# Performance work log

Measured on AMD Instinct MI355X. Metric: run time of the kernel, lower is better.

The kernel has to match this reference:

```python
import jax, jax.numpy as jnp
import numpy as np

D_MODEL = 1024
HEADS = 16
D_K = D_MODEL // HEADS
B, S = 2, 2048


def setup_inputs() -> dict:
    key = jax.random.key(0)
    ks = jax.random.split(key, 11)
    sc = 1.0 / np.sqrt(D_MODEL)
    inp = {
        "q": jax.random.normal(ks[0], (B, S, D_MODEL), jnp.float32),
        "k": jax.random.normal(ks[1], (B, S, D_MODEL), jnp.float32),
        "v": jax.random.normal(ks[2], (B, S, D_MODEL), jnp.float32),
        # causal mask, broadcastable to (B, H, S, S); 0 -> masked
        "mask": jnp.tril(jnp.ones((S, S), jnp.int32))[None, None],
        "w_q": jax.random.normal(ks[3], (D_MODEL, D_MODEL), jnp.float32) * sc,
        "b_q": jax.random.normal(ks[4], (D_MODEL,), jnp.float32) * sc,
        "w_k": jax.random.normal(ks[5], (D_MODEL, D_MODEL), jnp.float32) * sc,
        "b_k": jax.random.normal(ks[6], (D_MODEL,), jnp.float32) * sc,
        "w_v": jax.random.normal(ks[7], (D_MODEL, D_MODEL), jnp.float32) * sc,
        "b_v": jax.random.normal(ks[8], (D_MODEL,), jnp.float32) * sc,
        "w_o": jax.random.normal(ks[9], (D_MODEL, D_MODEL), jnp.float32) * sc,
        "b_o": jax.random.normal(ks[10], (D_MODEL,), jnp.float32) * sc,
    }
    return inp


def reference(q, k, v, mask, w_q, b_q, w_k, b_k, w_v, b_v, w_o, b_o):
    b = q.shape[0]
    # torch Linear: x @ W.T + b
    Q = q @ w_q.T + b_q
    K = k @ w_k.T + b_k
    V = v @ w_v.T + b_v
    # (B, S, D) -> (B, H, S, d_k)
    Q = Q.reshape(b, -1, HEADS, D_K).transpose(0, 2, 1, 3)
    K = K.reshape(b, -1, HEADS, D_K).transpose(0, 2, 1, 3)
    V = V.reshape(b, -1, HEADS, D_K).transpose(0, 2, 1, 3)
    scores = jnp.einsum("bhqd,bhkd->bhqk", Q, K) / np.sqrt(D_K).astype(np.float32)
    scores = jnp.where(mask == 0, -jnp.inf, scores)
    attn = jax.nn.softmax(scores, axis=-1)
    out = jnp.einsum("bhqk,bhkd->bhqd", attn, V)
    out = out.transpose(0, 2, 1, 3).reshape(b, -1, D_MODEL)
    # dropout is identity in eval mode
    return out @ w_o.T + b_o
```

## Files before the change

### kernel.cpp

```cpp
#include <hip/hip_runtime.h>
#include <math.h>

#define D_MODEL 1024
#define N_HEADS 16
#define DKH     64
#define BATCH   2
#define SEQ     2048
#define NT128   (SEQ/128)
#define PARTS_PER_BH 40

typedef unsigned short u16;
typedef __attribute__((ext_vector_type(8))) short short8;
typedef __attribute__((ext_vector_type(4))) float f32x4;

__device__ __forceinline__ u16 f2bf(float f) {
    unsigned u = __float_as_uint(f);
    u += 0x7fffu + ((u >> 16) & 1u);
    return (u16)(u >> 16);
}
__device__ __forceinline__ float bf2f(u16 x) {
    return __int_as_float(((int)x) << 16);
}

__device__ __forceinline__ void gll16(const void* g, void* l) {
    __builtin_amdgcn_global_load_lds((const __attribute__((address_space(1))) void*)g,
                                     (__attribute__((address_space(3))) void*)l, 16, 0, 0);
}

template<int CTRL>
__device__ __forceinline__ float rormax(float x) {
    int r = __builtin_amdgcn_update_dpp(__float_as_int(x), __float_as_int(x),
                                        CTRL, 0xf, 0xf, false);
    return fmaxf(x, __int_as_float(r));
}
__device__ __forceinline__ float rowmax16(float x) {
    x = rormax<0x121>(x);
    x = rormax<0x122>(x);
    x = rormax<0x124>(x);
    x = rormax<0x128>(x);
    return x;
}

__global__ __launch_bounds__(256)
void convert_kernel(const float* __restrict__ q, const float* __restrict__ k,
                    const float* __restrict__ v, const float* __restrict__ wq,
                    const float* __restrict__ wk, const float* __restrict__ wv,
                    const float* __restrict__ wo,
                    u16* __restrict__ qb, u16* __restrict__ kb, u16* __restrict__ vb,
                    u16* __restrict__ wqb, u16* __restrict__ wkb,
                    u16* __restrict__ wvb, u16* __restrict__ wob)
{
    const size_t NV = ((size_t)16 << 20) >> 3;
    for (size_t i = (size_t)blockIdx.x * blockDim.x + threadIdx.x; i < NV;
         i += (size_t)gridDim.x * blockDim.x) {
        const size_t e = i << 3;
        const float* s; u16* d; size_t off;
        if (e < ((size_t)12 << 20)) {
            const int seg = (int)(e >> 22);
            off = e & (((size_t)1 << 22) - 1);
            s = seg == 0 ? q : seg == 1 ? k : v;
            d = seg == 0 ? qb : seg == 1 ? kb : vb;
        } else {
            const size_t r = e - ((size_t)12 << 20);
            const int seg = (int)(r >> 20);
            off = r & (((size_t)1 << 20) - 1);
            s = seg == 0 ? wq : seg == 1 ? wk : seg == 2 ? wv : wo;
            d = seg == 0 ? wqb : seg == 1 ? wkb : seg == 2 ? wvb : wob;
        }
        const float4 f0 = *(const float4*)(s + off);
        const float4 f1 = *(const float4*)(s + off + 4);
        short8 o;
        o[0]=(short)f2bf(f0.x); o[1]=(short)f2bf(f0.y); o[2]=(short)f2bf(f0.z); o[3]=(short)f2bf(f0.w);
        o[4]=(short)f2bf(f1.x); o[5]=(short)f2bf(f1.y); o[6]=(short)f2bf(f1.z); o[7]=(short)f2bf(f1.w);
        *(short8*)(d + off) = o;
    }
}

#define GEMM_PREAMBLE                                                            \
    __shared__ __align__(16) u16 As[2][128][32];                                 \
    __shared__ __align__(16) u16 Bs[2][128][32];                                 \
    const int tid  = threadIdx.x;                                                \
    const int lane = tid & 63;                                                   \
    const int wid  = tid >> 6;                                                   \
    const int wm   = wid >> 1, wn = wid & 1;                                     \
    const int lr   = lane & 15, lg = lane >> 4;                                  \
    const int mb   = blockIdx.x * 128, nb = blockIdx.y * 128;                    \
    const int g_row = lane >> 2;                                                 \
    const int g_col = (lane & 3) << 3;                                           \
    const u16* Ab = A  + (size_t)mb * K;                                         \
    const u16* Bb = Bw + (size_t)nb * K;                                         \
    f32x4 acc[4][4];                                                             \
    _Pragma("unroll")                                                            \
    for (int i = 0; i < 4; ++i)                                                  \
        _Pragma("unroll")                                                        \
        for (int j = 0; j < 4; ++j) { f32x4 z = {0.f,0.f,0.f,0.f}; acc[i][j] = z; }

#define STAGE(buf, kt)                                                           \
    {                                                                            \
        _Pragma("unroll")                                                        \
        for (int t = 0; t < 2; ++t) {                                            \
            const int r0 = t*64 + wid*16;                                        \
            gll16(&Ab[(size_t)(r0 + g_row)*K + (kt) + g_col], &As[buf][r0][0]);  \
            gll16(&Bb[(size_t)(r0 + g_row)*K + (kt) + g_col], &Bs[buf][r0][0]);  \
        }                                                                        \
    }

#define GEMM_MAINLOOP                                                            \
    STAGE(0, 0)                                                                  \
    __syncthreads();                                                             \
    const int NK = K >> 5;                                                       \
    for (int it = 0; it < NK; ++it) {                                            \
        const int c = it & 1;                                                    \
        if (it + 1 < NK) STAGE(c ^ 1, (it + 1) << 5)                             \
        short8 a[4], b[4];                                                       \
        _Pragma("unroll")                                                        \
        for (int i = 0; i < 4; ++i) a[i] = *(const short8*)&As[c][wm*64 + i*16 + lr][lg*8]; \
        _Pragma("unroll")                                                        \
        for (int j = 0; j < 4; ++j) b[j] = *(const short8*)&Bs[c][wn*64 + j*16 + lr][lg*8]; \
        _Pragma("unroll")                                                        \
        for (int i = 0; i < 4; ++i)                                              \
            _Pragma("unroll")                                                    \
            for (int j = 0; j < 4; ++j)                                          \
                acc[i][j] = __builtin_amdgcn_mfma_f32_16x16x32_bf16(a[i], b[j], acc[i][j], 0, 0, 0); \
        __syncthreads();                                                         \
    }

__global__ __launch_bounds__(256, 3)
void gemm_qkv_kernel(const u16* __restrict__ qb, const u16* __restrict__ kb,
                     const u16* __restrict__ vb, const u16* __restrict__ wqb,
                     const u16* __restrict__ wkb, const u16* __restrict__ wvb,
                     const float* __restrict__ b_q, const float* __restrict__ b_k,
                     const float* __restrict__ b_v,
                     u16* __restrict__ Qh, u16* __restrict__ Kh, u16* __restrict__ Vt,
                     int M, int N, int K)
{
    const int z = blockIdx.z;
    const u16* A    = z == 0 ? qb  : z == 1 ? kb  : vb;
    const u16* Bw   = z == 0 ? wqb : z == 1 ? wkb : wvb;
    const float* bias = z == 0 ? b_q : z == 1 ? b_k : b_v;
    u16* dst        = z == 0 ? Qh  : z == 1 ? Kh  : Vt;
    const float scale = z == 0 ? 0.125f : 1.0f;

    GEMM_PREAMBLE
    GEMM_MAINLOOP

    #pragma unroll
    for (int i = 0; i < 4; ++i) {
        #pragma unroll
        for (int j = 0; j < 4; ++j) {
            const int mbase = mb + wm*64 + i*16 + lg*4;
            const int n     = nb + wn*64 + j*16 + lr;
            const float bn  = bias[n];
            const int h = n >> 6, d = n & 63;
            #pragma unroll
            for (int r = 0; r < 4; ++r) {
                const int m = mbase + r;
                const int b = m >> 11, s = m & (SEQ - 1);
                const float val = (acc[i][j][r] + bn) * scale;
                if (z == 2)
                    dst[(((size_t)(b*N_HEADS + h))*DKH + d)*SEQ + s] = f2bf(val);
                else
                    dst[(((size_t)(b*N_HEADS + h))*SEQ + s)*DKH + d] = f2bf(val);
            }
        }
    }
}

__global__ __launch_bounds__(256)
void gemm_out_kernel(const u16* __restrict__ A, const u16* __restrict__ Bw,
                     const float* __restrict__ bias, float* __restrict__ dst,
                     int M, int N, int K)
{
    __shared__ __align__(16) u16 As[2][128][32];
    __shared__ __align__(16) u16 Bs[2][64][32];

    const int tid  = threadIdx.x;
    const int lane = tid & 63;
    const int wid  = tid >> 6;
    const int wm   = wid >> 1, wn = wid & 1;
    const int lr   = lane & 15, lg = lane >> 4;
    const int mb   = blockIdx.x * 128, nb = blockIdx.y * 64;
    const int g_row = lane >> 2;
    const int g_col = (lane & 3) << 3;

    const u16* Ab = A  + (size_t)mb * K;
    const u16* Bb = Bw + (size_t)nb * K;

    f32x4 acc[4][2];
    #pragma unroll
    for (int i = 0; i < 4; ++i)
        #pragma unroll
        for (int j = 0; j < 2; ++j) { f32x4 z = {0.f,0.f,0.f,0.f}; acc[i][j] = z; }

#define OSTAGE(buf, kt)                                                          \
    {                                                                            \
        _Pragma("unroll")                                                        \
        for (int t = 0; t < 2; ++t) {                                            \
            const int r0 = t*64 + wid*16;                                        \
            gll16(&Ab[(size_t)(r0 + g_row)*K + (kt) + g_col], &As[buf][r0][0]);  \
        }                                                                        \
        gll16(&Bb[(size_t)(wid*16 + g_row)*K + (kt) + g_col], &Bs[buf][wid*16][0]); \
    }

    OSTAGE(0, 0)
    __syncthreads();

    const int NK = K >> 5;
    for (int it = 0; it < NK; ++it) {
        const int c = it & 1;
        if (it + 1 < NK) OSTAGE(c ^ 1, (it + 1) << 5)

        short8 a[4], b[2];
        #pragma unroll
        for (int i = 0; i < 4; ++i) a[i] = *(const short8*)&As[c][wm*64 + i*16 + lr][lg*8];
        #pragma unroll
        for (int j = 0; j < 2; ++j) b[j] = *(const short8*)&Bs[c][wn*32 + j*16 + lr][lg*8];
        #pragma unroll
        for (int i = 0; i < 4; ++i)
            #pragma unroll
            for (int j = 0; j < 2; ++j)
                acc[i][j] = __builtin_amdgcn_mfma_f32_16x16x32_bf16(a[i], b[j], acc[i][j], 0, 0, 0);

        __syncthreads();
    }
#undef OSTAGE

    #pragma unroll
    for (int i = 0; i < 4; ++i) {
        #pragma unroll
        for (int j = 0; j < 2; ++j) {
            const int mbase = mb + wm*64 + i*16 + lg*4;
            const int n     = nb + wn*32 + j*16 + lr;
            const float bn  = bias[n];
            #pragma unroll
            for (int r = 0; r < 4; ++r)
                dst[(size_t)(mbase + r) * N + n] = acc[i][j][r] + bn;
        }
    }
}

__device__ __forceinline__ void attn_step(
    const short8& aq0, const short8& aq1,
    f32x4 (&o)[4], f32x4& osum, float (&m_run)[4],
    const u16 (*__restrict__ Kl)[64], const u16 (*__restrict__ Vl)[64],
    u16 (*__restrict__ Pw)[72],
    int kvb, int qbw, int lr, int lg)
{
    const int ksw = (lr & 7) << 3;
    f32x4 s[4];
    __builtin_amdgcn_s_setprio(1);
    #pragma unroll
    for (int cb = 0; cb < 4; ++cb) {
        const int kr = cb*16 + lr;
        f32x4 z = {0.f,0.f,0.f,0.f};
        short8 k0 = *(const short8*)&Kl[kr][( 0 + lg*8) ^ ksw];
        short8 k1 = *(const short8*)&Kl[kr][(32 + lg*8) ^ ksw];
        z = __builtin_amdgcn_mfma_f32_16x16x32_bf16(aq0, k0, z, 0, 0, 0);
        z = __builtin_amdgcn_mfma_f32_16x16x32_bf16(aq1, k1, z, 0, 0, 0);
        s[cb] = z;
    }
    __builtin_amdgcn_s_setprio(0);

    if (kvb + 63 > qbw) {
        #pragma unroll
        for (int cb = 0; cb < 4; ++cb)
            #pragma unroll
            for (int r = 0; r < 4; ++r)
                if (kvb + cb*16 + lr > qbw + lg*4 + r) s[cb][r] = -INFINITY;
    }

    float tm[4];
    #pragma unroll
    for (int r = 0; r < 4; ++r)
        tm[r] = rowmax16(fmaxf(fmaxf(s[0][r], s[1][r]), fmaxf(s[2][r], s[3][r])));

    int need = 0;
    #pragma unroll
    for (int r = 0; r < 4; ++r) need |= (tm[r] > m_run[r] + 8.f) ? 1 : 0;
    if (__any(need)) {
        #pragma unroll
        for (int r = 0; r < 4; ++r) {
            const float mnew  = fmaxf(m_run[r], tm[r]);
            const float alpha = __expf(m_run[r] - mnew);
            m_run[r] = mnew;
            osum[r] *= alpha;
            #pragma unroll
            for (int db = 0; db < 4; ++db) o[db][r] *= alpha;
        }
    }
    #pragma unroll
    for (int r = 0; r < 4; ++r)
        #pragma unroll
        for (int cb = 0; cb < 4; ++cb)
            Pw[lg*4 + r][cb*16 + lr] = f2bf(__expf(s[cb][r] - m_run[r]));

    short8 vone;
    #pragma unroll
    for (int j = 0; j < 8; ++j) vone[j] = (short)0x3F80;
    __builtin_amdgcn_s_setprio(1);
    #pragma unroll
    for (int ks = 0; ks < 2; ++ks) {
        short8 ap = *(short8*)&Pw[lr][ks*32 + lg*8];
        #pragma unroll
        for (int db = 0; db < 4; ++db) {
            const int vr = db*16 + lr;
            short8 bv = *(const short8*)&Vl[vr][(ks*32 + lg*8) ^ ksw];
            o[db] = __builtin_amdgcn_mfma_f32_16x16x32_bf16(ap, bv, o[db], 0, 0, 0);
        }
        osum = __builtin_amdgcn_mfma_f32_16x16x32_bf16(ap, vone, osum, 0, 0, 0);
    }
    __builtin_amdgcn_s_setprio(0);
}

__global__ __launch_bounds__(512)
void flash_split_kernel(const u16* __restrict__ Qh, const u16* __restrict__ Kh,
                        const u16* __restrict__ Vt, u16* __restrict__ part_o,
                        float* __restrict__ part_ms)
{
    __shared__ __align__(16) u16 Kl[64][64];
    __shared__ __align__(16) u16 Vl[64][64];
    __shared__ __align__(16) u16 P[8][16][72];

    const int x = blockIdx.x;
    int t, ch;
    if      (x <  4) { t = x;                 ch = 0;        }
    else if (x < 12) { t = 4 + ((x-4) >> 1);  ch = (x-4)&1;  }
    else if (x < 24) { t = 8 + (x-12)/3;      ch = (x-12)%3; }
    else             { t = 12 + ((x-24) >> 2); ch = (x-24)&3; }

    const int tid  = threadIdx.x;
    const int lane = tid & 63;
    const int wid  = tid >> 6;
    const int lr   = lane & 15, lg = lane >> 4;
    const int bh   = blockIdx.y;
    const int qbw  = t*128 + wid*16;
    const size_t base = (size_t)bh * SEQ * DKH;

    const int c0      = ch * 8;
    const int nc_here = min(8, 2*(t+1) - c0);

    const int srow = tid >> 3;
    const int se0  = (tid & 7) << 3;
    const int sec  = se0 ^ ((srow & 7) << 3);

    short8 aq0 = *(const short8*)&Qh[base + (size_t)(qbw + lr)*DKH +  0 + lg*8];
    short8 aq1 = *(const short8*)&Qh[base + (size_t)(qbw + lr)*DKH + 32 + lg*8];

    f32x4 o[4], osum;
    float m_run[4];
    #pragma unroll
    for (int r = 0; r < 4; ++r) m_run[r] = -INFINITY;
    {
        f32x4 z = {0.f,0.f,0.f,0.f};
        osum = z;
        #pragma unroll
        for (int db = 0; db < 4; ++db) o[db] = z;
    }

    {
        const int kb0 = c0 * 64;
        short8 k0 = *(const short8*)&Kh[base + (size_t)(kb0 + srow)*DKH + se0];
        short8 v0 = *(const short8*)&Vt[base + (size_t)srow*SEQ + kb0 + se0];
        *(short8*)&Kl[srow][sec] = k0;
        *(short8*)&Vl[srow][sec] = v0;
    }
    __syncthreads();

    for (int ci = 0; ci < nc_here; ++ci) {
        const int kvb = (c0 + ci) * 64;
        short8 nk0, nv0;
        const bool pref = (ci + 1 < nc_here);
        if (pref) {
            const int nb_ = kvb + 64;
            nk0 = *(const short8*)&Kh[base + (size_t)(nb_ + srow)*DKH + se0];
            nv0 = *(const short8*)&Vt[base + (size_t)srow*SEQ + nb_ + se0];
        }

        if (kvb <= qbw + 15)
            attn_step(aq0, aq1, o, osum, m_run, Kl, Vl, P[wid], kvb, qbw, lr, lg);

        __syncthreads();
        if (pref) {
            *(short8*)&Kl[srow][sec] = nk0;
            *(short8*)&Vl[srow][sec] = nv0;
        }
        __syncthreads();
    }

    const size_t slot = (size_t)bh * PARTS_PER_BH + x;
    u16*   po = part_o  + (slot << 13);
    float* pm = part_ms + (slot << 8);
    #pragma unroll
    for (int db = 0; db < 4; ++db)
        #pragma unroll
        for (int r = 0; r < 4; ++r)
            po[(wid*16 + lg*4 + r)*64 + db*16 + lr] = f2bf(o[db][r]);
    if (lr == 0) {
        #pragma unroll
        for (int r = 0; r < 4; ++r) {
            pm[(wid*16 + lg*4 + r)*2 + 0] = m_run[r];
            pm[(wid*16 + lg*4 + r)*2 + 1] = osum[r];
        }
    }
}

__global__ __launch_bounds__(256)
void merge_kernel(const u16* __restrict__ part_o, const float* __restrict__ part_ms,
                  u16* __restrict__ attb)
{
    const int t   = blockIdx.x;
    const int bh  = blockIdx.y;
    const int nch = min(4, (2*(t+1) + 7) >> 3);
    const int basex = t < 4 ? t : t < 8 ? 4 + 2*(t-4) : t < 12 ? 12 + 3*(t-8) : 24 + 4*(t-12);

    const int row = threadIdx.x >> 1;
    const int cb  = (threadIdx.x & 1) * 32;

    float mm[4], ss[4];
    float M = -INFINITY;
    for (int c = 0; c < nch; ++c) {
        const size_t slot = (size_t)bh * PARTS_PER_BH + basex + c;
        mm[c] = part_ms[(slot << 8) + row*2 + 0];
        ss[c] = part_ms[(slot << 8) + row*2 + 1];
        M = fmaxf(M, mm[c]);
    }
    float S = 0.f;
    float acc[32];
    #pragma unroll
    for (int j = 0; j < 32; ++j) acc[j] = 0.f;
    for (int c = 0; c < nch; ++c) {
        const float w = __expf(mm[c] - M);
        S += w * ss[c];
        const size_t slot = (size_t)bh * PARTS_PER_BH + basex + c;
        const u16* po = part_o + (slot << 13) + row*64 + cb;
        #pragma unroll
        for (int g = 0; g < 4; ++g) {
            short8 v = *(const short8*)(po + g*8);
            #pragma unroll
            for (int j = 0; j < 8; ++j)
                acc[g*8 + j] += w * bf2f((u16)v[j]);
        }
    }
    const float inv = 1.f / S;
    const int b = bh >> 4, h = bh & 15;
    const int grow = t*128 + row;
    u16* dst = attb + ((size_t)(b*SEQ + grow))*D_MODEL + h*64 + cb;
    #pragma unroll
    for (int g = 0; g < 4; ++g) {
        short8 ov;
        #pragma unroll
        for (int j = 0; j < 8; ++j) ov[j] = (short)f2bf(acc[g*8 + j] * inv);
        *(short8*)(dst + g*8) = ov;
    }
}

extern "C" void kernel_launch(void* const* d_in, const int* in_sizes, int n_in,
                              void* d_out, int out_size, void* d_ws, size_t ws_size,
                              hipStream_t stream)
{
    const float* q   = (const float*)d_in[0];
    const float* k   = (const float*)d_in[1];
    const float* v   = (const float*)d_in[2];
    const float* w_q = (const float*)d_in[4];
    const float* b_q = (const float*)d_in[5];
    const float* w_k = (const float*)d_in[6];
    const float* b_k = (const float*)d_in[7];
    const float* w_v = (const float*)d_in[8];
    const float* b_v = (const float*)d_in[9];
    const float* w_o = (const float*)d_in[10];
    const float* b_o = (const float*)d_in[11];

    char* ws = (char*)d_ws;
    const size_t MB = 1024*1024;
    u16* Qh   = (u16*)(ws +  0*MB);
    u16* Kh   = (u16*)(ws +  8*MB);
    u16* Vt   = (u16*)(ws + 16*MB);
    u16* qb   = (u16*)(ws + 24*MB);
    u16* kb   = (u16*)(ws + 32*MB);
    u16* vb   = (u16*)(ws + 40*MB);
    u16* wqb  = (u16*)(ws + 48*MB);
    u16* wkb  = (u16*)(ws + 50*MB);
    u16* wvb  = (u16*)(ws + 52*MB);
    u16* wob  = (u16*)(ws + 54*MB);
    u16* attb = qb;
    u16*   part_o  = (u16*)(ws + 32*MB);
    float* part_ms = (float*)(ws + 52*MB);

    const int M = BATCH * SEQ, N = D_MODEL, K = D_MODEL;

    convert_kernel<<<2048, 256, 0, stream>>>(q, k, v, w_q, w_k, w_v, w_o,
                                             qb, kb, vb, wqb, wkb, wvb, wob);
    gemm_qkv_kernel<<<dim3(M/128, N/128, 3), 256, 0, stream>>>(
        qb, kb, vb, wqb, wkb, wvb, b_q, b_k, b_v, Qh, Kh, Vt, M, N, K);
    flash_split_kernel<<<dim3(PARTS_PER_BH, BATCH*N_HEADS), 512, 0, stream>>>(
        Qh, Kh, Vt, part_o, part_ms);
    merge_kernel<<<dim3(NT128, BATCH*N_HEADS), 256, 0, stream>>>(part_o, part_ms, attb);
    gemm_out_kernel<<<dim3(M/128, N/64), 256, 0, stream>>>(attb, wob, b_o, (float*)d_out, M, N, K);
}
```

Baseline: 139.8 us.

## Compute transposed S tile so P feeds PV MFMA from registers

The attention step now computes S transposed (K as the A operand), so each lane holds one query row's scores across 16 keys. This allows row max via two cross-lane shuffles and lets P be packed into bf16 registers with v_cvt_pk_bf16_f32, feeding 16x16x16 MFMAs directly instead of going through an LDS round trip. The row sum is accumulated in scalar FP32 instead of a ones-vector MFMA. In exchange it uses twice as many smaller-K PV MFMAs, needs shuffles to broadcast the rescale alpha, and loads V with 8-byte LDS reads.

```diff
diff --git a/kernel.cpp b/kernel.cpp
--- a/kernel.cpp
+++ b/kernel.cpp
@@ -10,7 +10,9 @@
 #define PARTS_PER_BH 40
 
 typedef unsigned short u16;
+typedef unsigned long long u64;
 typedef __attribute__((ext_vector_type(8))) short short8;
+typedef __attribute__((ext_vector_type(4))) short s4v;
 typedef __attribute__((ext_vector_type(4))) float f32x4;
 
 __device__ __forceinline__ u16 f2bf(float f) {
@@ -27,18 +29,16 @@
                                      (__attribute__((address_space(3))) void*)l, 16, 0, 0);
 }
 
-template<int CTRL>
-__device__ __forceinline__ float rormax(float x) {
-    int r = __builtin_amdgcn_update_dpp(__float_as_int(x), __float_as_int(x),
-                                        CTRL, 0xf, 0xf, false);
-    return fmaxf(x, __int_as_float(r));
-}
-__device__ __forceinline__ float rowmax16(float x) {
-    x = rormax<0x121>(x);
-    x = rormax<0x122>(x);
-    x = rormax<0x124>(x);
-    x = rormax<0x128>(x);
-    return x;
+__device__ __forceinline__ f32x4 mfma16(s4v a, s4v b, f32x4 c) {
+#if __has_builtin(__builtin_amdgcn_mfma_f32_16x16x16bf16_1k)
+    return __builtin_amdgcn_mfma_f32_16x16x16bf16_1k(a, b, c, 0, 0, 0);
+#elif __has_builtin(__builtin_amdgcn_mfma_f32_16x16x16_bf16)
+    return __builtin_amdgcn_mfma_f32_16x16x16_bf16(a, b, c, 0, 0, 0);
+#else
+    f32x4 d;
+    asm("v_mfma_f32_16x16x16_bf16 %0, %1, %2, %3" : "=v"(d) : "v"(a), "v"(b), "v"(c));
+    return d;
+#endif
 }
 
 __global__ __launch_bounds__(256)
@@ -241,73 +241,82 @@
 
 __device__ __forceinline__ void attn_step(
     const short8& aq0, const short8& aq1,
-    f32x4 (&o)[4], f32x4& osum, float (&m_run)[4],
+    f32x4 (&o)[4], float& osum, float& m_run,
     const u16 (*__restrict__ Kl)[64], const u16 (*__restrict__ Vl)[64],
-    u16 (*__restrict__ Pw)[72],
     int kvb, int qbw, int lr, int lg)
 {
     const int ksw = (lr & 7) << 3;
-    f32x4 s[4];
+    f32x4 st[4];
     __builtin_amdgcn_s_setprio(1);
     #pragma unroll
-    for (int cb = 0; cb < 4; ++cb) {
-        const int kr = cb*16 + lr;
+    for (int c = 0; c < 4; ++c) {
+        const int kr = c*16 + lr;
         f32x4 z = {0.f,0.f,0.f,0.f};
         short8 k0 = *(const short8*)&Kl[kr][( 0 + lg*8) ^ ksw];
         short8 k1 = *(const short8*)&Kl[kr][(32 + lg*8) ^ ksw];
-        z = __builtin_amdgcn_mfma_f32_16x16x32_bf16(aq0, k0, z, 0, 0, 0);
-        z = __builtin_amdgcn_mfma_f32_16x16x32_bf16(aq1, k1, z, 0, 0, 0);
-        s[cb] = z;
+        z = __builtin_amdgcn_mfma_f32_16x16x32_bf16(k0, aq0, z, 0, 0, 0);
+        z = __builtin_amdgcn_mfma_f32_16x16x32_bf16(k1, aq1, z, 0, 0, 0);
+        st[c] = z;
     }
     __builtin_amdgcn_s_setprio(0);
 
     if (kvb + 63 > qbw) {
         #pragma unroll
-        for (int cb = 0; cb < 4; ++cb)
+        for (int c = 0; c < 4; ++c)
             #pragma unroll
             for (int r = 0; r < 4; ++r)
-                if (kvb + cb*16 + lr > qbw + lg*4 + r) s[cb][r] = -INFINITY;
-    }
-
-    float tm[4];
-    #pragma unroll
-    for (int r = 0; r < 4; ++r)
-        tm[r] = rowmax16(fmaxf(fmaxf(s[0][r], s[1][r]), fmaxf(s[2][r], s[3][r])));
-
-    int need = 0;
-    #pragma unroll
-    for (int r = 0; r < 4; ++r) need |= (tm[r] > m_run[r] + 8.f) ? 1 : 0;
-    if (__any(need)) {
-        #pragma unroll
-        for (int r = 0; r < 4; ++r) {
-            const float mnew  = fmaxf(m_run[r], tm[r]);
-            const float alpha = __expf(m_run[r] - mnew);
-            m_run[r] = mnew;
-            osum[r] *= alpha;
+                if (kvb + c*16 + lg*4 + r > qbw + lr) st[c][r] = -INFINITY;
+    }
+
+    float tm = fmaxf(fmaxf(st[0][0], st[0][1]), fmaxf(st[0][2], st[0][3]));
+    #pragma unroll
+    for (int c = 1; c < 4; ++c)
+        tm = fmaxf(tm, fmaxf(fmaxf(st[c][0], st[c][1]), fmaxf(st[c][2], st[c][3])));
+    tm = fmaxf(tm, __shfl_xor(tm, 16));
+    tm = fmaxf(tm, __shfl_xor(tm, 32));
+
+    if (__any(tm > m_run + 8.f)) {
+        const float mnew  = fmaxf(m_run, tm);
+        const float alpha = __expf(m_run - mnew);
+        m_run = mnew;
+        osum *= alpha;
+        float af[4];
+        #pragma unroll
+        for (int r = 0; r < 4; ++r)
+            af[r] = __shfl(alpha, (lg << 4) | (lg*4 + r));
+        #pragma unroll
+        for (int db = 0; db < 4; ++db)
             #pragma unroll
-            for (int db = 0; db < 4; ++db) o[db][r] *= alpha;
-        }
-    }
-    #pragma unroll
-    for (int r = 0; r < 4; ++r)
-        #pragma unroll
-        for (int cb = 0; cb < 4; ++cb)
-            Pw[lg*4 + r][cb*16 + lr] = f2bf(__expf(s[cb][r] - m_run[r]));
-
-    short8 vone;
-    #pragma unroll
-    for (int j = 0; j < 8; ++j) vone[j] = (short)0x3F80;
+            for (int r = 0; r < 4; ++r) o[db][r] *= af[r];
+    }
+
+    s4v av[4];
+    float sum = 0.f;
+    #pragma unroll
+    for (int c = 0; c < 4; ++c) {
+        const float p0 = __expf(st[c][0] - m_run);
+        const float p1 = __expf(st[c][1] - m_run);
+        const float p2 = __expf(st[c][2] - m_run);
+        const float p3 = __expf(st[c][3] - m_run);
+        sum += (p0 + p1) + (p2 + p3);
+        unsigned lo, hi;
+        asm("v_cvt_pk_bf16_f32 %0, %1, %2" : "=v"(lo) : "v"(p0), "v"(p1));
+        asm("v_cvt_pk_bf16_f32 %0, %1, %2" : "=v"(hi) : "v"(p2), "v"(p3));
+        union { unsigned u[2]; s4v s; } uu;
+        uu.u[0] = lo; uu.u[1] = hi;
+        av[c] = uu.s;
+    }
+    osum += sum;
+
     __builtin_amdgcn_s_setprio(1);
     #pragma unroll
-    for (int ks = 0; ks < 2; ++ks) {
-        short8 ap = *(short8*)&Pw[lr][ks*32 + lg*8];
+    for (int c = 0; c < 4; ++c) {
         #pragma unroll
         for (int db = 0; db < 4; ++db) {
-            const int vr = db*16 + lr;
-            short8 bv = *(const short8*)&Vl[vr][(ks*32 + lg*8) ^ ksw];
-            o[db] = __builtin_amdgcn_mfma_f32_16x16x32_bf16(ap, bv, o[db], 0, 0, 0);
-        }
-        osum = __builtin_amdgcn_mfma_f32_16x16x32_bf16(ap, vone, osum, 0, 0, 0);
+            union { u64 q; s4v s; } bv;
+            bv.q = *(const u64*)&Vl[db*16 + lr][(c*16 + lg*4) ^ ksw];
+            o[db] = mfma16(av[c], bv.s, o[db]);
+        }
     }
     __builtin_amdgcn_s_setprio(0);
 }
@@ -319,7 +328,6 @@
 {
     __shared__ __align__(16) u16 Kl[64][64];
     __shared__ __align__(16) u16 Vl[64][64];
-    __shared__ __align__(16) u16 P[8][16][72];
 
     const int x = blockIdx.x;
     int t, ch;
@@ -346,13 +354,10 @@
     short8 aq0 = *(const short8*)&Qh[base + (size_t)(qbw + lr)*DKH +  0 + lg*8];
     short8 aq1 = *(const short8*)&Qh[base + (size_t)(qbw + lr)*DKH + 32 + lg*8];
 
-    f32x4 o[4], osum;
-    float m_run[4];
-    #pragma unroll
-    for (int r = 0; r < 4; ++r) m_run[r] = -INFINITY;
+    f32x4 o[4];
+    float osum = 0.f, m_run = -INFINITY;
     {
         f32x4 z = {0.f,0.f,0.f,0.f};
-        osum = z;
         #pragma unroll
         for (int db = 0; db < 4; ++db) o[db] = z;
     }
@@ -377,7 +382,7 @@
         }
 
         if (kvb <= qbw + 15)
-            attn_step(aq0, aq1, o, osum, m_run, Kl, Vl, P[wid], kvb, qbw, lr, lg);
+            attn_step(aq0, aq1, o, osum, m_run, Kl, Vl, kvb, qbw, lr, lg);
 
         __syncthreads();
         if (pref) {
@@ -387,6 +392,9 @@
         __syncthreads();
     }
 
+    osum += __shfl_xor(osum, 16);
+    osum += __shfl_xor(osum, 32);
+
     const size_t slot = (size_t)bh * PARTS_PER_BH + x;
     u16*   po = part_o  + (slot << 13);
     float* pm = part_ms + (slot << 8);
@@ -395,12 +403,9 @@
         #pragma unroll
         for (int r = 0; r < 4; ++r)
             po[(wid*16 + lg*4 + r)*64 + db*16 + lr] = f2bf(o[db][r]);
-    if (lr == 0) {
-        #pragma unroll
-        for (int r = 0; r < 4; ++r) {
-            pm[(wid*16 + lg*4 + r)*2 + 0] = m_run[r];
-            pm[(wid*16 + lg*4 + r)*2 + 1] = osum[r];
-        }
+    if (lane < 16) {
+        pm[(wid*16 + lane)*2 + 0] = m_run;
+        pm[(wid*16 + lane)*2 + 1] = osum;
     }
 }
 
```

After: 136.7 us. 1.02x faster.
